# Optimization experiments

Hardware: AMD Instinct MI355X
Metric: run time of the kernel (lower is better)

## Reference

```python
import jax, jax.numpy as jnp
import numpy as np

B = 1048576
L = 32

def setup_inputs() -> dict:
    key = jax.random.key(0)
    k1, k2 = jax.random.split(key)
    D_pred_logit = jax.random.normal(k1, (B, L), dtype=jnp.float32)
    # D is a true distribution over L bins: random positives normalized per row
    raw = jax.random.uniform(k2, (B, L), dtype=jnp.float32)
    D = raw / jnp.sum(raw, axis=1, keepdims=True)
    return {"D_pred_logit": D_pred_logit, "D": D}

def reference(D_pred_logit, D):
    Lc = D.shape[1]
    # Ordinal similarity matrix A[j,k] = 1 - |j-k|/(L-1)  (PSD by construction)
    idx = jnp.arange(Lc, dtype=jnp.float32)
    A = 1.0 - jnp.abs(idx[:, None] - idx[None, :]) / (Lc - 1)
    A = A.astype(D.dtype)
    Q = D - jax.nn.softmax(D_pred_logit, axis=1)  # [B, L]
    # mean(diag(Q @ A @ Q^T)) == mean over rows of sum((Q @ A) * Q, axis=1)
    # (same math; avoids the B x B intermediate of the original)
    per_row = jnp.sum((Q @ A) * Q, axis=1)  # [B]
    return jnp.mean(per_row)
```

## Files before the change

### kernel.cpp

```cpp
#include <hip/hip_runtime.h>


#define L_BINS  32
#define NTHREAD 256
#define NBLOCKS 1024
#define UNROLL  8

typedef float vfloat4 __attribute__((ext_vector_type(4)));

__global__ __launch_bounds__(NTHREAD) void qfd2_main(const float* __restrict__ logit,
                                                     const float* __restrict__ D,
                                                     float* __restrict__ partial,
                                                     int rows) {
    const int t    = threadIdx.x;
    const int lane = t & 63;
    const int s    = lane & 7;
    const int g    = lane >> 3;
    const int wid  = blockIdx.x * (NTHREAD / 64) + (t >> 6);
    const int nwaves = NBLOCKS * (NTHREAD / 64);

    const float w3 = (s == 7) ? 0.0f : 1.0f;

    float acc = 0.0f;

    for (int base = wid * 64; base < rows; base += nwaves * 64) {
        const size_t boff = (size_t)base * L_BINS + (size_t)(g * L_BINS + s * 4);
        const float* zp = logit + boff;
        const float* dp = D + boff;

        vfloat4 vz[UNROLL], vd[UNROLL];
#pragma unroll
        for (int u = 0; u < UNROLL; ++u) {
            vz[u] = *(const vfloat4*)(zp + u * (8 * L_BINS));
            vd[u] = *(const vfloat4*)(dp + u * (8 * L_BINS));
        }

#pragma unroll
        for (int u = 0; u < UNROLL; ++u) {
            const vfloat4 z = vz[u], d = vd[u];

            float m = fmaxf(fmaxf(z.x, z.y), fmaxf(z.z, z.w));
            m = fmaxf(m, __shfl_xor(m, 1, 8));
            m = fmaxf(m, __shfl_xor(m, 2, 8));
            m = fmaxf(m, __shfl_xor(m, 4, 8));

            const float e0 = __expf(z.x - m), e1 = __expf(z.y - m);
            const float e2 = __expf(z.z - m), e3 = __expf(z.w - m);
            float sum = (e0 + e1) + (e2 + e3);
            sum += __shfl_xor(sum, 1, 8);
            sum += __shfl_xor(sum, 2, 8);
            sum += __shfl_xor(sum, 4, 8);
            const float rs = 1.0f / sum;

            const float q0 = d.x - e0 * rs, q1 = d.y - e1 * rs;
            const float q2 = d.z - e2 * rs, q3 = d.w - e3 * rs;
            const float p0 = q0, p1 = p0 + q1, p2 = p1 + q2, p3 = p2 + q3;

            const float T = p3;
            float inc = T, tmp;
            tmp = __shfl_up(inc, 1, 8); if (s >= 1) inc += tmp;
            tmp = __shfl_up(inc, 2, 8); if (s >= 2) inc += tmp;
            tmp = __shfl_up(inc, 4, 8); if (s >= 4) inc += tmp;
            const float off_ = inc - T;
            const float S    = __shfl(inc, 7, 8);

            const float P0 = off_ + p0, P1 = off_ + p1;
            const float P2 = off_ + p2, P3 = off_ + p3;

            const float sPl  = ((P0 + P1) + P2) + w3 * P3;
            const float sP2l = fmaf(P0, P0, fmaf(P1, P1, fmaf(P2, P2, w3 * P3 * P3)));
            acc += (2.0f / 31.0f) * (sP2l - S * sPl) + 0.125f * (S * S);
        }
    }

#pragma unroll
    for (int msk = 1; msk < 64; msk <<= 1) acc += __shfl_xor(acc, msk);

    __shared__ float wpart[NTHREAD / 64];
    if ((t & 63) == 0) wpart[t >> 6] = acc;
    __syncthreads();
    if (t == 0)
        partial[blockIdx.x] = (wpart[0] + wpart[1]) + (wpart[2] + wpart[3]);
}

__global__ __launch_bounds__(256) void qfd2_fin(const float* __restrict__ partial,
                                                float* __restrict__ out,
                                                int nblocks, int rows) {
    double a = 0.0;
    for (int i = threadIdx.x; i < nblocks; i += 256) a += (double)partial[i];
#pragma unroll
    for (int msk = 1; msk < 64; msk <<= 1) a += __shfl_xor(a, msk);

    __shared__ double wp[4];
    if ((threadIdx.x & 63) == 0) wp[threadIdx.x >> 6] = a;
    __syncthreads();
    if (threadIdx.x == 0)
        out[0] = (float)(((wp[0] + wp[1]) + (wp[2] + wp[3])) / (double)rows);
}

extern "C" void kernel_launch(void* const* d_in, const int* in_sizes, int n_in,
                              void* d_out, int out_size, void* d_ws, size_t ws_size,
                              hipStream_t stream) {
    const float* logit = (const float*)d_in[0];
    const float* D     = (const float*)d_in[1];
    float* out         = (float*)d_out;
    float* partial     = (float*)d_ws;

    const int rows = in_sizes[0] / L_BINS;

    qfd2_main<<<NBLOCKS, NTHREAD, 0, stream>>>(logit, D, partial, rows);
    qfd2_fin<<<1, 256, 0, stream>>>(partial, out, NBLOCKS, rows);
}
```

Baseline: 278.3 us.

## Use inline-asm nontemporal buffer loads and double the grid size

Replaces the pointer-based vector loads with hand-written buffer_load_dwordx4 instructions that take a buffer resource descriptor, immediate offsets and streaming cache hints (sc0 sc1 nt), followed by an explicit wait for all loads and a scheduling barrier. The grid is also doubled to 2048 blocks to put more waves in flight. The aim is fewer address-computation instructions and less cache pollution on a purely streaming read. In exchange, the full vmcnt(0) wait blocks any overlap between this batch's loads and compute, and 32-bit offsets cap the addressable size.

```diff
diff --git a/kernel.cpp b/kernel.cpp
--- a/kernel.cpp
+++ b/kernel.cpp
@@ -3,10 +3,26 @@
 
 #define L_BINS  32
 #define NTHREAD 256
-#define NBLOCKS 1024
+#define NBLOCKS 2048
 #define UNROLL  8
 
 typedef float vfloat4 __attribute__((ext_vector_type(4)));
+typedef unsigned int uint4v __attribute__((ext_vector_type(4)));
+
+__device__ __forceinline__ uint4v make_srd(const void* p) {
+    union { const void* p; unsigned long long u; } a; a.p = p;
+    uint4v d;
+    d.x = (unsigned)(a.u & 0xFFFFFFFFu);
+    d.y = (unsigned)(a.u >> 32);
+    d.z = 0xFFFFFFFFu;
+    d.w = 0x00020000u;
+    return d;
+}
+
+#define BLOAD(dst, srd, voff, IMM)                                              \
+    asm volatile("buffer_load_dwordx4 %0, %1, %2, 0 offen offset:" #IMM         \
+                 " sc0 sc1 nt"                                                  \
+                 : "=v"(dst) : "v"(voff), "s"(srd))
 
 __global__ __launch_bounds__(NTHREAD) void qfd2_main(const float* __restrict__ logit,
                                                      const float* __restrict__ D,
@@ -19,21 +35,36 @@
     const int wid  = blockIdx.x * (NTHREAD / 64) + (t >> 6);
     const int nwaves = NBLOCKS * (NTHREAD / 64);
 
+    const uint4v srdZ = make_srd(logit);
+    const uint4v srdD = make_srd(D);
+
     const float w3 = (s == 7) ? 0.0f : 1.0f;
 
     float acc = 0.0f;
 
     for (int base = wid * 64; base < rows; base += nwaves * 64) {
-        const size_t boff = (size_t)base * L_BINS + (size_t)(g * L_BINS + s * 4);
-        const float* zp = logit + boff;
-        const float* dp = D + boff;
+        const unsigned voff0 = (unsigned)(base + g) * 128u + (unsigned)(s * 16);
+        const unsigned voff1 = voff0 + 4096u;
 
         vfloat4 vz[UNROLL], vd[UNROLL];
-#pragma unroll
-        for (int u = 0; u < UNROLL; ++u) {
-            vz[u] = *(const vfloat4*)(zp + u * (8 * L_BINS));
-            vd[u] = *(const vfloat4*)(dp + u * (8 * L_BINS));
-        }
+        BLOAD(vz[0], srdZ, voff0, 0);
+        BLOAD(vz[1], srdZ, voff0, 1024);
+        BLOAD(vz[2], srdZ, voff0, 2048);
+        BLOAD(vz[3], srdZ, voff0, 3072);
+        BLOAD(vz[4], srdZ, voff1, 0);
+        BLOAD(vz[5], srdZ, voff1, 1024);
+        BLOAD(vz[6], srdZ, voff1, 2048);
+        BLOAD(vz[7], srdZ, voff1, 3072);
+        BLOAD(vd[0], srdD, voff0, 0);
+        BLOAD(vd[1], srdD, voff0, 1024);
+        BLOAD(vd[2], srdD, voff0, 2048);
+        BLOAD(vd[3], srdD, voff0, 3072);
+        BLOAD(vd[4], srdD, voff1, 0);
+        BLOAD(vd[5], srdD, voff1, 1024);
+        BLOAD(vd[6], srdD, voff1, 2048);
+        BLOAD(vd[7], srdD, voff1, 3072);
+        asm volatile("s_waitcnt vmcnt(0)" ::: "memory");
+        __builtin_amdgcn_sched_barrier(0);
 
 #pragma unroll
         for (int u = 0; u < UNROLL; ++u) {
```

New measurement: 249.9 us. -10.2%, faster.
